# Optimization experiments

Hardware: AMD Instinct MI355X
Metric: run time of the kernel (lower is better)

## Reference

```python
import jax, jax.numpy as jnp
import numpy as np

NUM_NODE = 100000
DEG = 16
E = NUM_NODE * DEG
IN_C = 128
HID_C = 128
NUM_REL = 8


def setup_inputs() -> dict:
    key = jax.random.key(0)
    k1, k2, k3, k4, k5, k6 = jax.random.split(key, 6)
    x = jax.random.normal(k1, (NUM_NODE, IN_C), dtype=jnp.float32)
    # glorot-style init for relation weights [num_rel, in, hid]
    scale = jnp.sqrt(6.0 / (IN_C + HID_C)).astype(jnp.float32)
    rel_weight = jax.random.uniform(k2, (NUM_REL, IN_C, HID_C), dtype=jnp.float32, minval=-1.0, maxval=1.0) * scale
    # uniform-degree CSR so every node has deg >= 1 (avoids div-by-zero, matches module assumption)
    ptr = jnp.arange(NUM_NODE + 1, dtype=jnp.int64) * DEG
    idx = jax.random.randint(k3, (E,), 0, NUM_NODE, dtype=jnp.int64)
    edge_types = jax.random.randint(k4, (E,), 0, NUM_REL, dtype=jnp.int64)
    # about 1/3 of nodes have cached history (value != -1)
    history_map = jax.random.randint(k5, (NUM_NODE,), -1, 2, dtype=jnp.int64)
    history_buffer = jax.random.normal(k6, (NUM_NODE, HID_C), dtype=jnp.float32)
    return {
        'x': x,
        'rel_weight': rel_weight,
        'ptr': ptr,
        'idx': idx,
        'edge_types': edge_types,
        'history_map': history_map,
        'history_buffer': history_buffer,
        'history_size': 1,
        'num_node': NUM_NODE,
    }


def reference(x, rel_weight, ptr, idx, edge_types, history_map, history_buffer, history_size, num_node):
    E_ = idx.shape[0]
    num_rel = rel_weight.shape[0]
    hid = rel_weight.shape[2]
    xg = x[idx]                                   # [E, in] gather of source features
    # relation-grouped transform: small static loop over relations, masked accumulate
    msgs = jnp.zeros((E_, hid), dtype=x.dtype)
    for r in range(num_rel):
        msgs = msgs + jnp.where((edge_types == r)[:, None], xg @ rel_weight[r], jnp.zeros((), x.dtype))
    deg = ptr[1:] - ptr[:-1]                      # [num_node]
    seg = jnp.repeat(jnp.arange(num_node), deg, total_repeat_length=E_)  # dst id per edge
    out = jax.ops.segment_sum(msgs, seg, num_segments=num_node)          # scatter-sum
    out = out / deg[:, None].astype(out.dtype)    # degree normalization
    if history_size > 0:                          # static python int
        out = jnp.where((history_map != -1)[:, None], history_buffer, out)
    return (out, out)
```

## Files before the change

kernel.cpp:

```cpp
#include <hip/hip_runtime.h>
#include <stdint.h>

#define IN_C   128
#define HID_C  128
#define NREL   8
#define K_TOTAL (NREL * IN_C)
#define TILE_M  16
#define SRB     1032

typedef float  f32x4  __attribute__((ext_vector_type(4)));
typedef __bf16 bf16x8 __attribute__((ext_vector_type(8)));
typedef short  s16x8  __attribute__((ext_vector_type(8)));
typedef unsigned short u16;

__device__ __forceinline__ unsigned short f2bf(float f) {
    unsigned int u = __float_as_uint(f);
    u += 0x7fffu + ((u >> 16) & 1u);
    return (unsigned short)(u >> 16);
}

__global__ void zero_count_kernel(unsigned int* count) { *count = 0u; }

__global__ __launch_bounds__(256) void prep_kernel(
        const float* __restrict__ W, const int* __restrict__ hmap,
        unsigned short* __restrict__ Wt, int* __restrict__ list,
        unsigned int* __restrict__ count, int NN, int WE) {
    int tid = blockIdx.x * blockDim.x + threadIdx.x;

    bool active = (tid < NN) && (hmap[tid] == -1);
    unsigned long long mask = __ballot(active);
    if (mask) {
        int lane   = threadIdx.x & 63;
        int leader = __ffsll((unsigned long long)mask) - 1;
        unsigned base = 0;
        if (lane == leader) base = atomicAdd(count, (unsigned)__popcll(mask));
        base = __shfl(base, leader, 64);
        if (active) {
            int off = __popcll(mask & ((1ull << lane) - 1ull));
            list[base + off] = tid;
        }
    }

    if (tid < WE) {
        int r   = tid >> 14;
        int rem = tid & 16383;
        int k   = rem >> 7;
        int c   = rem & 127;
        Wt[(size_t)c * K_TOTAL + r * IN_C + k] = f2bf(W[tid]);
    }
}

__global__ __launch_bounds__(256) void history_kernel(
        const int* __restrict__ hmap, const float* __restrict__ hbuf,
        float* __restrict__ out, int NN) {
    int gid = blockIdx.x * blockDim.x + threadIdx.x;
    int n = gid >> 5;
    int q = gid & 31;
    if (n >= NN) return;
    if (hmap[n] != -1) {
        const f32x4* src = (const f32x4*)hbuf;
        f32x4 v = src[(size_t)n * 32 + q];
        f32x4* o = (f32x4*)out;
        o[(size_t)n * 32 + q] = v;
        o[(size_t)NN * 32 + (size_t)n * 32 + q] = v;
    }
}

__global__ __launch_bounds__(256, 3) void gemm_kernel(
        const float* __restrict__ x,
        const int* __restrict__ ptr,
        const int* __restrict__ idx,
        const int* __restrict__ ety,
        const unsigned short* __restrict__ Wt,
        const int* __restrict__ list,
        const unsigned int* __restrict__ count,
        float* __restrict__ out, int NN) {
    __shared__ u16      S[TILE_M * SRB];
    __shared__ unsigned meta[TILE_M * 16];
    __shared__ int      nids[TILE_M];
    __shared__ int      degs[TILE_M];
    __shared__ float    invdeg[TILE_M];

    unsigned int cnt = *count;
    int rowbase = blockIdx.x * TILE_M;
    if (rowbase >= (int)cnt) return;

    int t = threadIdx.x;
    if (t < TILE_M) {
        int row = rowbase + t;
        int nid = -1, d = 0; float idg = 0.f;
        if (row < (int)cnt) {
            nid = list[row];
            int e0 = ptr[nid], e1 = ptr[nid + 1];
            d = e1 - e0;
            idg = (d > 0) ? 1.0f / (float)d : 0.f;
        }
        nids[t] = nid; degs[t] = d; invdeg[t] = idg;
    }
    __syncthreads();

    int n = t >> 4;
    int c = t & 15;
    int nid = nids[n];
    int deg = degs[n];
    int e0  = (nid >= 0) ? ptr[nid] : 0;

    int maxdeg = 0;
    #pragma unroll
    for (int i = 0; i < TILE_M; ++i) maxdeg = max(maxdeg, degs[i]);

    f32x4 alo[NREL], ahi[NREL];
    #pragma unroll
    for (int r = 0; r < NREL; ++r) { alo[r] = f32x4{0,0,0,0}; ahi[r] = f32x4{0,0,0,0}; }

    const float* xc = x + c * 8;

    for (int jb = 0; jb < maxdeg; jb += 16) {
        {
            int j = jb + c;
            unsigned m = 0xFFFFFFFFu;
            if (nid >= 0 && j < deg) {
                int e = e0 + j;
                m = ((unsigned)idx[e]) | (((unsigned)ety[e]) << 27);
            }
            meta[t] = m;
        }
        __syncthreads();

        unsigned mm[16];
        {
            uint4 q0 = *(const uint4*)(meta + (n << 4) + 0);
            uint4 q1 = *(const uint4*)(meta + (n << 4) + 4);
            uint4 q2 = *(const uint4*)(meta + (n << 4) + 8);
            uint4 q3 = *(const uint4*)(meta + (n << 4) + 12);
            mm[0]=q0.x;  mm[1]=q0.y;  mm[2]=q0.z;  mm[3]=q0.w;
            mm[4]=q1.x;  mm[5]=q1.y;  mm[6]=q1.z;  mm[7]=q1.w;
            mm[8]=q2.x;  mm[9]=q2.y;  mm[10]=q2.z; mm[11]=q2.w;
            mm[12]=q3.x; mm[13]=q3.y; mm[14]=q3.z; mm[15]=q3.w;
        }
        int offs[16];
        int rel[16];
        #pragma unroll
        for (int j = 0; j < 16; ++j) {
            unsigned m = mm[j];
            bool valid = (m != 0xFFFFFFFFu);
            int src = valid ? (int)(m & 0x07FFFFFFu) : 0;
            rel[j]  = valid ? (int)(m >> 27) : 31;
            offs[j] = src * IN_C;
        }

        f32x4 blo[4], bhi[4];
        #pragma unroll
        for (int u = 0; u < 4; ++u) {
            const f32x4* p = (const f32x4*)(xc + offs[u]);
            blo[u] = p[0]; bhi[u] = p[1];
        }
        #pragma unroll
        for (int b = 0; b < 4; ++b) {
            f32x4 nlo[4], nhi[4];
            if (b < 3) {
                #pragma unroll
                for (int u = 0; u < 4; ++u) {
                    const f32x4* p = (const f32x4*)(xc + offs[(b + 1) * 4 + u]);
                    nlo[u] = p[0]; nhi[u] = p[1];
                }
            }
            #pragma unroll
            for (int u = 0; u < 4; ++u) {
                int r = rel[b * 4 + u];
                #pragma unroll
                for (int rr = 0; rr < NREL; ++rr) {
                    float mk = (r == rr) ? 1.0f : 0.0f;
                    alo[rr] += blo[u] * mk;
                    ahi[rr] += bhi[u] * mk;
                }
            }
            if (b < 3) {
                #pragma unroll
                for (int u = 0; u < 4; ++u) { blo[u] = nlo[u]; bhi[u] = nhi[u]; }
            }
        }
        __syncthreads();
    }

    {
        u16* srow = S + n * SRB + c * 8;
        #pragma unroll
        for (int rr = 0; rr < NREL; ++rr) {
            s16x8 pk;
            pk[0] = (short)f2bf(alo[rr][0]); pk[1] = (short)f2bf(alo[rr][1]);
            pk[2] = (short)f2bf(alo[rr][2]); pk[3] = (short)f2bf(alo[rr][3]);
            pk[4] = (short)f2bf(ahi[rr][0]); pk[5] = (short)f2bf(ahi[rr][1]);
            pk[6] = (short)f2bf(ahi[rr][2]); pk[7] = (short)f2bf(ahi[rr][3]);
            *(s16x8*)(srow + rr * IN_C) = pk;
        }
    }
    __syncthreads();

    int wave = t >> 6, lane = t & 63;
    int quad = lane >> 4, l16 = lane & 15;
    int chbase = wave * 32;
    const u16* arow  = S + l16 * SRB + quad * 8;
    const u16* bbase = Wt + (size_t)(chbase + l16) * K_TOTAL + quad * 8;

    f32x4 acc0 = {0.f,0.f,0.f,0.f};
    f32x4 acc1 = {0.f,0.f,0.f,0.f};
    #pragma unroll 8
    for (int ks = 0; ks < K_TOTAL; ks += 32) {
        s16x8 a  = *(const s16x8*)(arow + ks);
        s16x8 b0 = *(const s16x8*)(bbase + ks);
        s16x8 b1 = *(const s16x8*)(bbase + ks + 16 * K_TOTAL);
        union { s16x8 s; bf16x8 b; } ua, ub0, ub1;
        ua.s = a; ub0.s = b0; ub1.s = b1;
        acc0 = __builtin_amdgcn_mfma_f32_16x16x32_bf16(ua.b, ub0.b, acc0, 0, 0, 0);
        acc1 = __builtin_amdgcn_mfma_f32_16x16x32_bf16(ua.b, ub1.b, acc1, 0, 0, 0);
    }

    size_t half = (size_t)NN * HID_C;
    #pragma unroll
    for (int v = 0; v < 4; ++v) {
        int rowl = quad * 4 + v;
        int onid = nids[rowl];
        if (onid < 0) continue;
        float s = invdeg[rowl];
        float v0 = acc0[v] * s;
        float v1 = acc1[v] * s;
        size_t o0 = (size_t)onid * HID_C + chbase + l16;
        out[o0]             = v0;
        out[o0 + 16]        = v1;
        out[o0 + half]      = v0;
        out[o0 + 16 + half] = v1;
    }
}

extern "C" void kernel_launch(void* const* d_in, const int* in_sizes, int n_in,
                              void* d_out, int out_size, void* d_ws, size_t ws_size,
                              hipStream_t stream) {
    const float* x    = (const float*)d_in[0];
    const float* W    = (const float*)d_in[1];
    const int*   ptr  = (const int*)d_in[2];
    const int*   idx  = (const int*)d_in[3];
    const int*   ety  = (const int*)d_in[4];
    const int*   hmap = (const int*)d_in[5];
    const float* hbuf = (const float*)d_in[6];
    int NN = in_sizes[5];
    int WE = in_sizes[1];
    float* out = (float*)d_out;

    unsigned int* count = (unsigned int*)d_ws;
    int* list = (int*)((char*)d_ws + 256);
    size_t wt_off = 256 + (((size_t)NN * 4 + 4095) / 4096) * 4096;
    unsigned short* Wt = (unsigned short*)((char*)d_ws + wt_off);

    zero_count_kernel<<<1, 1, 0, stream>>>(count);

    int total = WE > NN ? WE : NN;
    prep_kernel<<<(total + 255) / 256, 256, 0, stream>>>(W, hmap, Wt, list, count, NN, WE);
    history_kernel<<<((size_t)NN * 32 + 255) / 256, 256, 0, stream>>>(hmap, hbuf, out, NN);
    gemm_kernel<<<(NN + TILE_M - 1) / TILE_M, 256, 0, stream>>>(
        x, ptr, idx, ety, Wt, list, count, out, NN);
}
```

Measured before the change: 299.6 us.

## Gather bf16 copy of node features and fuse history copy into prep kernel

Adds a pre-pass that converts x to bf16 in workspace, so the per-edge gather in the aggregation kernel reads half the bytes. The history copy kernel is merged into the prep kernel, which removes one launch. The aggregation kernel's launch bounds go from 3 to 4 waves, and the invalid-edge sentinel is simplified to relation 31. The cost is an extra pass that reads x and writes a bf16 copy each call, plus the precision loss from rounding the gathered features before aggregation. The fp32 path is kept as a fallback when the workspace is too small.

```diff
diff --git a/kernel.cpp b/kernel.cpp
--- a/kernel.cpp
+++ b/kernel.cpp
@@ -22,52 +22,60 @@
 __global__ void zero_count_kernel(unsigned int* count) { *count = 0u; }
 
 __global__ __launch_bounds__(256) void prep_kernel(
-        const float* __restrict__ W, const int* __restrict__ hmap,
-        unsigned short* __restrict__ Wt, int* __restrict__ list,
-        unsigned int* __restrict__ count, int NN, int WE) {
-    int tid = blockIdx.x * blockDim.x + threadIdx.x;
-
-    bool active = (tid < NN) && (hmap[tid] == -1);
-    unsigned long long mask = __ballot(active);
-    if (mask) {
-        int lane   = threadIdx.x & 63;
-        int leader = __ffsll((unsigned long long)mask) - 1;
-        unsigned base = 0;
-        if (lane == leader) base = atomicAdd(count, (unsigned)__popcll(mask));
-        base = __shfl(base, leader, 64);
-        if (active) {
-            int off = __popcll(mask & ((1ull << lane) - 1ull));
-            list[base + off] = tid;
-        }
-    }
-
-    if (tid < WE) {
-        int r   = tid >> 14;
-        int rem = tid & 16383;
+        const float* __restrict__ x, const float* __restrict__ W,
+        const int* __restrict__ hmap, const float* __restrict__ hbuf,
+        unsigned short* __restrict__ xh, unsigned short* __restrict__ Wt,
+        int* __restrict__ list, unsigned int* __restrict__ count,
+        float* __restrict__ out, int NN, int WE, int use_xh) {
+    int gid = blockIdx.x * blockDim.x + threadIdx.x;
+
+    {
+        bool active = (gid < NN) && (hmap[gid] == -1);
+        unsigned long long mask = __ballot(active);
+        if (mask) {
+            int lane   = threadIdx.x & 63;
+            int leader = __ffsll((unsigned long long)mask) - 1;
+            unsigned base = 0;
+            if (lane == leader) base = atomicAdd(count, (unsigned)__popcll(mask));
+            base = __shfl(base, leader, 64);
+            if (active) {
+                int off = __popcll(mask & ((1ull << lane) - 1ull));
+                list[base + off] = gid;
+            }
+        }
+    }
+
+    int n = gid >> 5;
+    int q = gid & 31;
+    if (n < NN) {
+        if (use_xh) {
+            f32x4 xv = ((const f32x4*)x)[(size_t)n * 32 + q];
+            ushort4 pk;
+            pk.x = f2bf(xv[0]); pk.y = f2bf(xv[1]);
+            pk.z = f2bf(xv[2]); pk.w = f2bf(xv[3]);
+            ((ushort4*)xh)[(size_t)n * 32 + q] = pk;
+        }
+        if (hmap[n] != -1) {
+            f32x4 v = ((const f32x4*)hbuf)[(size_t)n * 32 + q];
+            f32x4* o = (f32x4*)out;
+            o[(size_t)n * 32 + q] = v;
+            o[(size_t)NN * 32 + (size_t)n * 32 + q] = v;
+        }
+    }
+
+    if (gid < WE) {
+        int r   = gid >> 14;
+        int rem = gid & 16383;
         int k   = rem >> 7;
         int c   = rem & 127;
-        Wt[(size_t)c * K_TOTAL + r * IN_C + k] = f2bf(W[tid]);
+        Wt[(size_t)c * K_TOTAL + r * IN_C + k] = f2bf(W[gid]);
     }
 }
 
-__global__ __launch_bounds__(256) void history_kernel(
-        const int* __restrict__ hmap, const float* __restrict__ hbuf,
-        float* __restrict__ out, int NN) {
-    int gid = blockIdx.x * blockDim.x + threadIdx.x;
-    int n = gid >> 5;
-    int q = gid & 31;
-    if (n >= NN) return;
-    if (hmap[n] != -1) {
-        const f32x4* src = (const f32x4*)hbuf;
-        f32x4 v = src[(size_t)n * 32 + q];
-        f32x4* o = (f32x4*)out;
-        o[(size_t)n * 32 + q] = v;
-        o[(size_t)NN * 32 + (size_t)n * 32 + q] = v;
-    }
-}
-
-__global__ __launch_bounds__(256, 3) void gemm_kernel(
+template<int XBF>
+__global__ __launch_bounds__(256, 4) void gemm_kernel_t(
         const float* __restrict__ x,
+        const unsigned short* __restrict__ xh,
         const int* __restrict__ ptr,
         const int* __restrict__ idx,
         const int* __restrict__ ety,
@@ -113,12 +121,41 @@
     #pragma unroll
     for (int r = 0; r < NREL; ++r) { alo[r] = f32x4{0,0,0,0}; ahi[r] = f32x4{0,0,0,0}; }
 
-    const float* xc = x + c * 8;
+    const char* xcb = XBF ? ((const char*)xh + c * 16)
+                          : ((const char*)x  + c * 32);
+
+    auto accum_bf = [&](uint4 v, unsigned m) {
+        int r_ = (int)(m >> 27);
+        f32x4 lo_, hi_;
+        lo_[0] = __uint_as_float(v.x << 16);
+        lo_[1] = __uint_as_float(v.x & 0xFFFF0000u);
+        lo_[2] = __uint_as_float(v.y << 16);
+        lo_[3] = __uint_as_float(v.y & 0xFFFF0000u);
+        hi_[0] = __uint_as_float(v.z << 16);
+        hi_[1] = __uint_as_float(v.z & 0xFFFF0000u);
+        hi_[2] = __uint_as_float(v.w << 16);
+        hi_[3] = __uint_as_float(v.w & 0xFFFF0000u);
+        #pragma unroll
+        for (int rr = 0; rr < NREL; ++rr) {
+            float mk = (r_ == rr) ? 1.0f : 0.0f;
+            alo[rr] += lo_ * mk;
+            ahi[rr] += hi_ * mk;
+        }
+    };
+    auto accum_f32 = [&](f32x4 lo_, f32x4 hi_, unsigned m) {
+        int r_ = (int)(m >> 27);
+        #pragma unroll
+        for (int rr = 0; rr < NREL; ++rr) {
+            float mk = (r_ == rr) ? 1.0f : 0.0f;
+            alo[rr] += lo_ * mk;
+            ahi[rr] += hi_ * mk;
+        }
+    };
 
     for (int jb = 0; jb < maxdeg; jb += 16) {
         {
             int j = jb + c;
-            unsigned m = 0xFFFFFFFFu;
+            unsigned m = 31u << 27;
             if (nid >= 0 && j < deg) {
                 int e = e0 + j;
                 m = ((unsigned)idx[e]) | (((unsigned)ety[e]) << 27);
@@ -138,46 +175,50 @@
             mm[8]=q2.x;  mm[9]=q2.y;  mm[10]=q2.z; mm[11]=q2.w;
             mm[12]=q3.x; mm[13]=q3.y; mm[14]=q3.z; mm[15]=q3.w;
         }
-        int offs[16];
-        int rel[16];
-        #pragma unroll
-        for (int j = 0; j < 16; ++j) {
-            unsigned m = mm[j];
-            bool valid = (m != 0xFFFFFFFFu);
-            int src = valid ? (int)(m & 0x07FFFFFFu) : 0;
-            rel[j]  = valid ? (int)(m >> 27) : 31;
-            offs[j] = src * IN_C;
-        }
-
-        f32x4 blo[4], bhi[4];
-        #pragma unroll
-        for (int u = 0; u < 4; ++u) {
-            const f32x4* p = (const f32x4*)(xc + offs[u]);
-            blo[u] = p[0]; bhi[u] = p[1];
-        }
-        #pragma unroll
-        for (int b = 0; b < 4; ++b) {
-            f32x4 nlo[4], nhi[4];
-            if (b < 3) {
+
+        if (XBF) {
+            uint4 cur[4];
+            #pragma unroll
+            for (int u = 0; u < 4; ++u)
+                cur[u] = *(const uint4*)(xcb + ((size_t)(mm[u] & 0x07FFFFFFu) << 8));
+            #pragma unroll
+            for (int b = 0; b < 4; ++b) {
+                uint4 nxt[4];
+                if (b < 3) {
+                    #pragma unroll
+                    for (int u = 0; u < 4; ++u)
+                        nxt[u] = *(const uint4*)(xcb + ((size_t)(mm[(b+1)*4+u] & 0x07FFFFFFu) << 8));
+                }
                 #pragma unroll
-                for (int u = 0; u < 4; ++u) {
-                    const f32x4* p = (const f32x4*)(xc + offs[(b + 1) * 4 + u]);
-                    nlo[u] = p[0]; nhi[u] = p[1];
+                for (int u = 0; u < 4; ++u) accum_bf(cur[u], mm[b*4+u]);
+                if (b < 3) {
+                    #pragma unroll
+                    for (int u = 0; u < 4; ++u) cur[u] = nxt[u];
                 }
             }
+        } else {
+            f32x4 clo[4], chi[4];
             #pragma unroll
             for (int u = 0; u < 4; ++u) {
-                int r = rel[b * 4 + u];
+                const f32x4* p = (const f32x4*)(xcb + ((size_t)(mm[u] & 0x07FFFFFFu) << 9));
+                clo[u] = p[0]; chi[u] = p[1];
+            }
+            #pragma unroll
+            for (int b = 0; b < 4; ++b) {
+                f32x4 nlo[4], nhi[4];
+                if (b < 3) {
+                    #pragma unroll
+                    for (int u = 0; u < 4; ++u) {
+                        const f32x4* p = (const f32x4*)(xcb + ((size_t)(mm[(b+1)*4+u] & 0x07FFFFFFu) << 9));
+                        nlo[u] = p[0]; nhi[u] = p[1];
+                    }
+                }
                 #pragma unroll
-                for (int rr = 0; rr < NREL; ++rr) {
-                    float mk = (r == rr) ? 1.0f : 0.0f;
-                    alo[rr] += blo[u] * mk;
-                    ahi[rr] += bhi[u] * mk;
+                for (int u = 0; u < 4; ++u) accum_f32(clo[u], chi[u], mm[b*4+u]);
+                if (b < 3) {
+                    #pragma unroll
+                    for (int u = 0; u < 4; ++u) { clo[u] = nlo[u]; chi[u] = nhi[u]; }
                 }
-            }
-            if (b < 3) {
-                #pragma unroll
-                for (int u = 0; u < 4; ++u) { blo[u] = nlo[u]; bhi[u] = nhi[u]; }
             }
         }
         __syncthreads();
@@ -251,12 +292,24 @@
     int* list = (int*)((char*)d_ws + 256);
     size_t wt_off = 256 + (((size_t)NN * 4 + 4095) / 4096) * 4096;
     unsigned short* Wt = (unsigned short*)((char*)d_ws + wt_off);
+    size_t xh_off = ((wt_off + (size_t)K_TOTAL * HID_C * 2 + 4095) / 4096) * 4096;
+    unsigned short* xh = (unsigned short*)((char*)d_ws + xh_off);
+    size_t need = xh_off + (size_t)NN * IN_C * 2;
+    int use_xh = (ws_size >= need) ? 1 : 0;
 
     zero_count_kernel<<<1, 1, 0, stream>>>(count);
 
-    int total = WE > NN ? WE : NN;
-    prep_kernel<<<(total + 255) / 256, 256, 0, stream>>>(W, hmap, Wt, list, count, NN, WE);
-    history_kernel<<<((size_t)NN * 32 + 255) / 256, 256, 0, stream>>>(hmap, hbuf, out, NN);
-    gemm_kernel<<<(NN + TILE_M - 1) / TILE_M, 256, 0, stream>>>(
-        x, ptr, idx, ety, Wt, list, count, out, NN);
+    long long tot = (long long)NN * 32;
+    if (tot < (long long)WE) tot = WE;
+    prep_kernel<<<(int)((tot + 255) / 256), 256, 0, stream>>>(
+        x, W, hmap, hbuf, xh, Wt, list, count, out, NN, WE, use_xh);
+
+    int gblocks = (NN + TILE_M - 1) / TILE_M;
+    if (use_xh) {
+        gemm_kernel_t<1><<<gblocks, 256, 0, stream>>>(
+            x, xh, ptr, idx, ety, Wt, list, count, out, NN);
+    } else {
+        gemm_kernel_t<0><<<gblocks, 256, 0, stream>>>(
+            x, xh, ptr, idx, ety, Wt, list, count, out, NN);
+    }
 }
```

Measured after the change: 300.7 us. About the same (+0.4%).
